# Kernel optimization log

Measured on AMD Instinct MI355X. Metric: run time of the kernel, lower is better.

The kernel has to match this reference:

```python
import jax, jax.numpy as jnp
import numpy as np

UNITS = 128
FILTERS = 32
KSIZE = 31
B, T, DV, DQ = 64, 1000, 512, 1024


def setup_inputs() -> dict:
    key = jax.random.key(0)
    ks = jax.random.split(key, 12)
    scale = 0.05
    inp = {
        "query": jax.random.normal(ks[0], (B, DQ), jnp.float32),
        "values": jax.random.normal(ks[1], (B, T, DV), jnp.float32),
        "previous_attention_weights": jax.random.uniform(ks[2], (B, T, 1), jnp.float32),
        # learned params
        "Wq": jax.random.normal(ks[3], (DQ, UNITS), jnp.float32) * scale,
        "bq": jnp.zeros((UNITS,), jnp.float32),
        "Wm": jax.random.normal(ks[4], (DV, UNITS), jnp.float32) * scale,
        "bm": jnp.zeros((UNITS,), jnp.float32),
        "Wv": jax.random.normal(ks[5], (UNITS, 1), jnp.float32) * scale,
        "bv": jnp.zeros((1,), jnp.float32),
        "Wconv": jax.random.normal(ks[6], (KSIZE, 1, FILTERS), jnp.float32) * scale,  # [W, Cin, Cout]
        "Wl": jax.random.normal(ks[7], (FILTERS, UNITS), jnp.float32) * scale,
    }
    return inp


def _forward(query, values, prev_w, Wq, bq, Wm, bm, Wv, bv, Wconv, Wl):
    # location features: Conv1D (same padding, no bias) then Dense(tanh, no bias)
    loc = jax.lax.conv_general_dilated(
        prev_w, Wconv, window_strides=(1,), padding="SAME",
        dimension_numbers=("NWC", "WIO", "NWC"))          # [B, T, FILTERS]
    loc = jnp.tanh(loc @ Wl)                                # [B, T, UNITS]
    q = query @ Wq + bq                                     # [B, UNITS]
    m = values @ Wm + bm                                    # [B, T, UNITS]
    score = jnp.tanh(m + q[:, None, :] + loc) @ Wv + bv     # [B, T, 1]
    attention_weights = jax.nn.softmax(score, axis=1)       # softmax over time
    context = jnp.sum(attention_weights * values, axis=1)   # [B, DV]
    return context, attention_weights


def reference(query, values, previous_attention_weights, Wq, bq, Wm, bm, Wv, bv, Wconv, Wl):
    return _forward(query, values, previous_attention_weights,
                    Wq, bq, Wm, bm, Wv, bv, Wconv, Wl)
```

## Files before the change

### kernel.cpp

```cpp
#include <hip/hip_runtime.h>

#define B_  64
#define T_  1000
#define DV_ 512
#define DQ_ 1024
#define U_  128
#define F_  32
#define KS_ 31
#define P_  16
#define CT_ 63

typedef __attribute__((ext_vector_type(8))) short short8;
typedef __attribute__((ext_vector_type(4))) float f32x4;

__device__ __forceinline__ unsigned pk2(float a, float b) {
    union { float f; unsigned u; } x, y;
    x.f = a; y.f = b;
    unsigned ra = (x.u + 0x7FFFu + ((x.u >> 16) & 1u)) >> 16;
    unsigned rb = (y.u + 0x7FFFu + ((y.u >> 16) & 1u)) >> 16;
    return (ra & 0xFFFFu) | (rb << 16);
}

__device__ __forceinline__ float fast_tanh(float x) {
    return 1.0f - 2.0f / (__expf(2.0f * x) + 1.0f);
}

__device__ __forceinline__ short8 pk8(float4 f0, float4 f1) {
    int4 q;
    q.x = pk2(f0.x, f0.y); q.y = pk2(f0.z, f0.w);
    q.z = pk2(f1.x, f1.y); q.w = pk2(f1.z, f1.w);
    return *(short8*)&q;
}

__global__ __launch_bounds__(1024) void prep_qb_kernel(
    const float* __restrict__ Wm, const float* __restrict__ Wl,
    const float* __restrict__ query, const float* __restrict__ Wq,
    const float* __restrict__ bq, const float* __restrict__ bm,
    short* __restrict__ WmX, short* __restrict__ WlX, float* __restrict__ qb)
{
    __shared__ float sh[DQ_ + 8 * U_];
    int blk = blockIdx.x, tid = threadIdx.x;
    if (blk < 9) {
        int g = blk * 1024 + tid;
        if (g < 8192) {
            int kc = g >> 9, e = g & 511;
            int n = e >> 2, q = e & 3;
            int kb = kc * 32 + q * 8;
            int4 p;
            p.x = pk2(Wm[(kb + 0) * U_ + n], Wm[(kb + 1) * U_ + n]);
            p.y = pk2(Wm[(kb + 2) * U_ + n], Wm[(kb + 3) * U_ + n]);
            p.z = pk2(Wm[(kb + 4) * U_ + n], Wm[(kb + 5) * U_ + n]);
            p.w = pk2(Wm[(kb + 6) * U_ + n], Wm[(kb + 7) * U_ + n]);
            ((int4*)WmX)[g] = p;
        } else if (g < 8704) {
            int e = g - 8192;
            int n = e >> 2, q = e & 3;
            int kb = q * 8;
            int4 p;
            p.x = pk2(Wl[(kb + 0) * U_ + n], Wl[(kb + 1) * U_ + n]);
            p.y = pk2(Wl[(kb + 2) * U_ + n], Wl[(kb + 3) * U_ + n]);
            p.z = pk2(Wl[(kb + 4) * U_ + n], Wl[(kb + 5) * U_ + n]);
            p.w = pk2(Wl[(kb + 6) * U_ + n], Wl[(kb + 7) * U_ + n]);
            ((int4*)WlX)[e] = p;
        }
    } else {
        float* qs = sh;
        float* red = sh + DQ_;
        int b = blk - 9;
        qs[tid] = query[b * DQ_ + tid];
        __syncthreads();
        int u = tid & 127, p = tid >> 7;
        float a = 0.f;
        const float* wp = Wq + (size_t)p * 128 * U_ + u;
        const float* qp = qs + p * 128;
#pragma unroll 8
        for (int k = 0; k < 128; ++k) a += qp[k] * wp[(size_t)k * U_];
        red[p * U_ + u] = a;
        __syncthreads();
        if (tid < U_) {
            float s = bq[tid] + bm[tid];
#pragma unroll
            for (int pp = 0; pp < 8; ++pp) s += red[pp * U_ + tid];
            qb[b * U_ + tid] = s;
        }
    }
}

__global__ __launch_bounds__(256) void score_kernel(
    const float* __restrict__ values, const float* __restrict__ prev,
    const float* __restrict__ Wc, const float* __restrict__ Wv,
    const float* __restrict__ bv, const short* __restrict__ WmX,
    const short* __restrict__ WlX, const float* __restrict__ qb,
    float* __restrict__ scores)
{
    __shared__ float WcS[KS_ * F_];
    __shared__ short AsL[128 * 32];
    __shared__ float qbS[2 * U_];
    __shared__ float WvS[U_];

    const int tid = threadIdx.x;
    const int r0 = blockIdx.x * 128;
    const int b0 = r0 / T_;
    const int b1 = (r0 + 127) / T_;

    for (int i = tid; i < KS_ * F_; i += 256) WcS[i] = Wc[i];
    if (tid < U_) WvS[tid] = Wv[tid];
    {
        int bb = (tid < U_) ? b0 : b1;
        qbS[tid] = qb[bb * U_ + (tid & (U_ - 1))];
    }

    const int wv = tid >> 6, lane = tid & 63;
    const int quad = lane >> 4, m15 = lane & 15;
    const int row0 = wv * 32 + m15;
    const float* aP0 = values + (size_t)(r0 + row0) * DV_ + quad * 8;
    const float* aP1 = aP0 + (size_t)16 * DV_;
    const int4* bW  = (const int4*)WmX + m15 * 4 + quad;
    const int4* blW = (const int4*)WlX + m15 * 4 + quad;

    float4 aq0[2][2], aq1[2][2], aq2[2][2];
    int4 bf0[8], bf1[8];
    aq0[0][0] = *(const float4*)(aP0);      aq0[0][1] = *(const float4*)(aP0 + 4);
    aq0[1][0] = *(const float4*)(aP1);      aq0[1][1] = *(const float4*)(aP1 + 4);
    aq1[0][0] = *(const float4*)(aP0 + 32); aq1[0][1] = *(const float4*)(aP0 + 36);
    aq1[1][0] = *(const float4*)(aP1 + 32); aq1[1][1] = *(const float4*)(aP1 + 36);
#pragma unroll
    for (int c = 0; c < 8; ++c) bf0[c] = bW[c * 64];

    __syncthreads();

#pragma unroll
    for (int it = 0; it < 2; ++it) {
        int idx = tid + it * 256;
        int i = idx & 127, fg = idx >> 7;
        int r = r0 + i;
        int b = r / T_;
        int t = r - b * T_;
        const float* pv = prev + b * T_;
        float a8[8] = {};
#pragma unroll
        for (int k = 0; k < KS_; ++k) {
            int tt = t + k - 15;
            float p = ((unsigned)tt < (unsigned)T_) ? pv[tt] : 0.f;
#pragma unroll
            for (int j = 0; j < 8; ++j) a8[j] += p * WcS[k * F_ + fg * 8 + j];
        }
        int4 pq;
        pq.x = pk2(a8[0], a8[1]); pq.y = pk2(a8[2], a8[3]);
        pq.z = pk2(a8[4], a8[5]); pq.w = pk2(a8[6], a8[7]);
        ((int4*)AsL)[i * 4 + (fg ^ ((i >> 1) & 3))] = pq;
    }
    __syncthreads();

    f32x4 acc[2][8] = {};
    {
        int row1 = row0 + 16;
        short8 afl0 = ((const short8*)AsL)[row0 * 4 + (quad ^ ((row0 >> 1) & 3))];
        short8 afl1 = ((const short8*)AsL)[row1 * 4 + (quad ^ ((row1 >> 1) & 3))];
#pragma unroll
        for (int c = 0; c < 8; ++c) {
            int4 bl = blW[c * 64];
            acc[0][c] = __builtin_amdgcn_mfma_f32_16x16x32_bf16(afl0, *(short8*)&bl, acc[0][c], 0, 0, 0);
            acc[1][c] = __builtin_amdgcn_mfma_f32_16x16x32_bf16(afl1, *(short8*)&bl, acc[1][c], 0, 0, 0);
        }
        int qoff[2][4];
#pragma unroll
        for (int g = 0; g < 2; ++g)
#pragma unroll
            for (int v = 0; v < 4; ++v) {
                int r = r0 + wv * 32 + g * 16 + quad * 4 + v;
                qoff[g][v] = ((r / T_) == b0) ? 0 : U_;
            }
#pragma unroll
        for (int g = 0; g < 2; ++g)
#pragma unroll
            for (int c = 0; c < 8; ++c) {
                int col = c * 16 + m15;
#pragma unroll
                for (int v = 0; v < 4; ++v)
                    acc[g][c][v] = qbS[qoff[g][v] + col] + fast_tanh(acc[g][c][v]);
            }
    }

#pragma unroll
    for (int kc = 0; kc < 16; ++kc) {
        if (kc + 2 < 16) {
            aq2[0][0] = *(const float4*)(aP0 + (kc + 2) * 32);
            aq2[0][1] = *(const float4*)(aP0 + (kc + 2) * 32 + 4);
            aq2[1][0] = *(const float4*)(aP1 + (kc + 2) * 32);
            aq2[1][1] = *(const float4*)(aP1 + (kc + 2) * 32 + 4);
        }
        if (kc + 1 < 16) {
#pragma unroll
            for (int c = 0; c < 8; ++c) bf1[c] = bW[(kc + 1) * 512 + c * 64];
        }
        short8 af0 = pk8(aq0[0][0], aq0[0][1]);
        short8 af1 = pk8(aq0[1][0], aq0[1][1]);
#pragma unroll
        for (int c = 0; c < 8; ++c) {
            acc[0][c] = __builtin_amdgcn_mfma_f32_16x16x32_bf16(af0, *(short8*)&bf0[c], acc[0][c], 0, 0, 0);
            acc[1][c] = __builtin_amdgcn_mfma_f32_16x16x32_bf16(af1, *(short8*)&bf0[c], acc[1][c], 0, 0, 0);
        }
#pragma unroll
        for (int g = 0; g < 2; ++g) {
            aq0[g][0] = aq1[g][0]; aq0[g][1] = aq1[g][1];
            aq1[g][0] = aq2[g][0]; aq1[g][1] = aq2[g][1];
        }
#pragma unroll
        for (int c = 0; c < 8; ++c) bf0[c] = bf1[c];
    }

    float psum[2][4] = {};
#pragma unroll
    for (int g = 0; g < 2; ++g)
#pragma unroll
        for (int c = 0; c < 8; ++c) {
            int col = c * 16 + m15;
            float wvv = WvS[col];
#pragma unroll
            for (int v = 0; v < 4; ++v)
                psum[g][v] += fast_tanh(acc[g][c][v]) * wvv;
        }
#pragma unroll
    for (int off = 1; off < 16; off <<= 1) {
#pragma unroll
        for (int g = 0; g < 2; ++g)
#pragma unroll
            for (int v = 0; v < 4; ++v) psum[g][v] += __shfl_xor(psum[g][v], off);
    }
    if (m15 == 0) {
        float bvv = bv[0];
#pragma unroll
        for (int g = 0; g < 2; ++g)
#pragma unroll
            for (int v = 0; v < 4; ++v)
                scores[r0 + wv * 32 + g * 16 + quad * 4 + v] = psum[g][v] + bvv;
    }
}

__global__ void softmax_kernel(const float* __restrict__ s, float* __restrict__ w) {
    __shared__ float red[4];
    int b = blockIdx.x, tid = threadIdx.x;
    const float* sb = s + b * T_;
    float v[4];
    int tv[4];
#pragma unroll
    for (int i = 0; i < 4; ++i) {
        int t = tid + i * 256;
        tv[i] = t;
        v[i] = (t < T_) ? sb[t] : -1e30f;
    }
    float mx = fmaxf(fmaxf(v[0], v[1]), fmaxf(v[2], v[3]));
#pragma unroll
    for (int off = 32; off >= 1; off >>= 1) mx = fmaxf(mx, __shfl_xor(mx, off));
    int wv = tid >> 6, lane = tid & 63;
    if (lane == 0) red[wv] = mx;
    __syncthreads();
    mx = fmaxf(fmaxf(red[0], red[1]), fmaxf(red[2], red[3]));
    float e[4];
    float sum = 0.f;
#pragma unroll
    for (int i = 0; i < 4; ++i) {
        e[i] = (tv[i] < T_) ? __expf(v[i] - mx) : 0.f;
        sum += e[i];
    }
#pragma unroll
    for (int off = 32; off >= 1; off >>= 1) sum += __shfl_xor(sum, off);
    __syncthreads();
    if (lane == 0) red[wv] = sum;
    __syncthreads();
    sum = red[0] + red[1] + red[2] + red[3];
    float inv = 1.0f / sum;
#pragma unroll
    for (int i = 0; i < 4; ++i)
        if (tv[i] < T_) w[b * T_ + tv[i]] = e[i] * inv;
}

__global__ __launch_bounds__(256) void ctx1_kernel(
    const float* __restrict__ values, const float* __restrict__ w,
    float* __restrict__ part)
{
    __shared__ float wS[CT_];
    __shared__ float4 ps[128];
    int b = blockIdx.x, p = blockIdx.y, tid = threadIdx.x;
    int t0 = p * CT_;
    int len = (T_ - t0 < CT_) ? (T_ - t0) : CT_;
    if (tid < len) wS[tid] = w[b * T_ + t0 + tid];
    __syncthreads();
    int cl = tid & 127, tp = tid >> 7;
    const float* vp = values + ((size_t)b * T_ + t0) * DV_ + cl * 4;
    float4 a = {0.f, 0.f, 0.f, 0.f};
#pragma unroll 4
    for (int t = tp; t < len; t += 2) {
        float4 v = *(const float4*)(vp + (size_t)t * DV_);
        float wt = wS[t];
        a.x += wt * v.x; a.y += wt * v.y; a.z += wt * v.z; a.w += wt * v.w;
    }
    if (tp == 1) ps[cl] = a;
    __syncthreads();
    if (tp == 0) {
        float4 o = ps[cl];
        o.x += a.x; o.y += a.y; o.z += a.z; o.w += a.w;
        *(float4*)(part + ((size_t)(b * P_ + p)) * DV_ + cl * 4) = o;
    }
}

__global__ void ctx2_kernel(const float* __restrict__ part, float* __restrict__ ctx) {
    int b = blockIdx.x, tid = threadIdx.x;
    const float* pp = part + (size_t)b * P_ * DV_ + tid * 4;
    float4 s = {0.f, 0.f, 0.f, 0.f};
#pragma unroll
    for (int p = 0; p < P_; ++p) {
        float4 v = *(const float4*)(pp + (size_t)p * DV_);
        s.x += v.x; s.y += v.y; s.z += v.z; s.w += v.w;
    }
    *(float4*)(ctx + (size_t)b * DV_ + tid * 4) = s;
}

extern "C" void kernel_launch(void* const* d_in, const int* in_sizes, int n_in,
                              void* d_out, int out_size, void* d_ws, size_t ws_size,
                              hipStream_t stream) {
    const float* query  = (const float*)d_in[0];
    const float* values = (const float*)d_in[1];
    const float* prev   = (const float*)d_in[2];
    const float* Wq     = (const float*)d_in[3];
    const float* bq     = (const float*)d_in[4];
    const float* Wm     = (const float*)d_in[5];
    const float* bm     = (const float*)d_in[6];
    const float* Wv     = (const float*)d_in[7];
    const float* bv     = (const float*)d_in[8];
    const float* Wc     = (const float*)d_in[9];
    const float* Wl     = (const float*)d_in[10];

    float* out  = (float*)d_out;
    float* ctx  = out;
    float* attw = out + B_ * DV_;

    char* ws = (char*)d_ws;
    float* qb     = (float*)(ws);
    float* scores = (float*)(ws + 32768);
    short* WmX    = (short*)(ws + 288768);
    short* WlX    = (short*)(ws + 419840);
    float* part   = (float*)(ws + 428032);

    prep_qb_kernel<<<73, 1024, 0, stream>>>(Wm, Wl, query, Wq, bq, bm, WmX, WlX, qb);
    score_kernel<<<500, 256, 0, stream>>>(values, prev, Wc, Wv, bv, WmX, WlX, qb, scores);
    softmax_kernel<<<B_, 256, 0, stream>>>(scores, attw);
    ctx1_kernel<<<dim3(B_, P_), 256, 0, stream>>>(values, attw, part);
    ctx2_kernel<<<B_, 128, 0, stream>>>(part, ctx);
}
```

Measured before the change: 272.8 us.

## Stage values via global_load_lds double buffer, halve score tile, fuse softmax into context

The score kernel now covers 64 rows per block instead of 128 and runs 1000 blocks with a launch bound of 3 blocks per CU. It streams the values operand into a double-buffered LDS tile with async global_load_lds and a swizzled layout, replacing the per-lane register prefetch. The softmax kernel is folded into the first context kernel: each (batch, chunk) block recomputes the max and sum over all scores, then computes its own weights inline, which removes one launch and one round trip of the weights. The price is redundant softmax reductions in every block, more LDS per block, and a syncthreads each k-step.

```diff
diff --git a/kernel.cpp b/kernel.cpp
--- a/kernel.cpp
+++ b/kernel.cpp
@@ -30,6 +30,12 @@
     q.x = pk2(f0.x, f0.y); q.y = pk2(f0.z, f0.w);
     q.z = pk2(f1.x, f1.y); q.w = pk2(f1.z, f1.w);
     return *(short8*)&q;
+}
+
+__device__ __forceinline__ void gload_lds16(const void* g, void* l) {
+    __builtin_amdgcn_global_load_lds(
+        (const __attribute__((address_space(1))) unsigned*)g,
+        (__attribute__((address_space(3))) unsigned*)l, 16, 0, 0);
 }
 
 __global__ __launch_bounds__(1024) void prep_qb_kernel(
@@ -86,22 +92,46 @@
     }
 }
 
-__global__ __launch_bounds__(256) void score_kernel(
+__global__ __launch_bounds__(256, 3) void score_kernel(
     const float* __restrict__ values, const float* __restrict__ prev,
     const float* __restrict__ Wc, const float* __restrict__ Wv,
     const float* __restrict__ bv, const short* __restrict__ WmX,
     const short* __restrict__ WlX, const float* __restrict__ qb,
     float* __restrict__ scores)
 {
+    __shared__ float As[2][64 * 64];
+    __shared__ short AsL[64 * 32];
     __shared__ float WcS[KS_ * F_];
-    __shared__ short AsL[128 * 32];
     __shared__ float qbS[2 * U_];
     __shared__ float WvS[U_];
 
     const int tid = threadIdx.x;
-    const int r0 = blockIdx.x * 128;
+    const int r0 = blockIdx.x * 64;
     const int b0 = r0 / T_;
-    const int b1 = (r0 + 127) / T_;
+    const int b1 = (r0 + 63) / T_;
+
+    const int wv = tid >> 6, lane = tid & 63;
+    const int quad = lane >> 4, m15 = lane & 15;
+    const int esw = (m15 & 3) << 1;
+    const int lrow = lane >> 4;
+    const int lunit = (lane & 15) ^ (lrow << 1);
+
+    const int4* bW  = (const int4*)WmX + m15 * 4 + quad;
+    const int4* blW = (const int4*)WlX + m15 * 4 + quad;
+
+    auto stage = [&](int buf, int k0) {
+#pragma unroll
+        for (int j = 0; j < 4; ++j) {
+            const float* src = values + (size_t)(r0 + wv * 16 + j * 4 + lrow) * DV_
+                               + k0 + lunit * 4;
+            gload_lds16(src, &As[buf][(wv * 16 + j * 4) * 64]);
+        }
+    };
+
+    stage(0, 0);
+    int4 bfA[8], bfB[8];
+#pragma unroll
+    for (int c = 0; c < 8; ++c) bfA[c] = bW[c * 64];
 
     for (int i = tid; i < KS_ * F_; i += 256) WcS[i] = Wc[i];
     if (tid < U_) WvS[tid] = Wv[tid];
@@ -109,30 +139,10 @@
         int bb = (tid < U_) ? b0 : b1;
         qbS[tid] = qb[bb * U_ + (tid & (U_ - 1))];
     }
-
-    const int wv = tid >> 6, lane = tid & 63;
-    const int quad = lane >> 4, m15 = lane & 15;
-    const int row0 = wv * 32 + m15;
-    const float* aP0 = values + (size_t)(r0 + row0) * DV_ + quad * 8;
-    const float* aP1 = aP0 + (size_t)16 * DV_;
-    const int4* bW  = (const int4*)WmX + m15 * 4 + quad;
-    const int4* blW = (const int4*)WlX + m15 * 4 + quad;
-
-    float4 aq0[2][2], aq1[2][2], aq2[2][2];
-    int4 bf0[8], bf1[8];
-    aq0[0][0] = *(const float4*)(aP0);      aq0[0][1] = *(const float4*)(aP0 + 4);
-    aq0[1][0] = *(const float4*)(aP1);      aq0[1][1] = *(const float4*)(aP1 + 4);
-    aq1[0][0] = *(const float4*)(aP0 + 32); aq1[0][1] = *(const float4*)(aP0 + 36);
-    aq1[1][0] = *(const float4*)(aP1 + 32); aq1[1][1] = *(const float4*)(aP1 + 36);
-#pragma unroll
-    for (int c = 0; c < 8; ++c) bf0[c] = bW[c * 64];
-
-    __syncthreads();
-
-#pragma unroll
-    for (int it = 0; it < 2; ++it) {
-        int idx = tid + it * 256;
-        int i = idx & 127, fg = idx >> 7;
+    __syncthreads();
+
+    {
+        int i = tid & 63, fg = tid >> 6;
         int r = r0 + i;
         int b = r / T_;
         int t = r - b * T_;
@@ -152,149 +162,132 @@
     }
     __syncthreads();
 
-    f32x4 acc[2][8] = {};
+    const int row = wv * 16 + m15;
+    f32x4 acc[8] = {};
     {
-        int row1 = row0 + 16;
-        short8 afl0 = ((const short8*)AsL)[row0 * 4 + (quad ^ ((row0 >> 1) & 3))];
-        short8 afl1 = ((const short8*)AsL)[row1 * 4 + (quad ^ ((row1 >> 1) & 3))];
+        short8 afl = ((const short8*)AsL)[row * 4 + (quad ^ ((row >> 1) & 3))];
 #pragma unroll
         for (int c = 0; c < 8; ++c) {
             int4 bl = blW[c * 64];
-            acc[0][c] = __builtin_amdgcn_mfma_f32_16x16x32_bf16(afl0, *(short8*)&bl, acc[0][c], 0, 0, 0);
-            acc[1][c] = __builtin_amdgcn_mfma_f32_16x16x32_bf16(afl1, *(short8*)&bl, acc[1][c], 0, 0, 0);
-        }
-        int qoff[2][4];
-#pragma unroll
-        for (int g = 0; g < 2; ++g)
-#pragma unroll
-            for (int v = 0; v < 4; ++v) {
-                int r = r0 + wv * 32 + g * 16 + quad * 4 + v;
-                qoff[g][v] = ((r / T_) == b0) ? 0 : U_;
-            }
-#pragma unroll
-        for (int g = 0; g < 2; ++g)
-#pragma unroll
-            for (int c = 0; c < 8; ++c) {
-                int col = c * 16 + m15;
-#pragma unroll
-                for (int v = 0; v < 4; ++v)
-                    acc[g][c][v] = qbS[qoff[g][v] + col] + fast_tanh(acc[g][c][v]);
-            }
-    }
-
-#pragma unroll
-    for (int kc = 0; kc < 16; ++kc) {
-        if (kc + 2 < 16) {
-            aq2[0][0] = *(const float4*)(aP0 + (kc + 2) * 32);
-            aq2[0][1] = *(const float4*)(aP0 + (kc + 2) * 32 + 4);
-            aq2[1][0] = *(const float4*)(aP1 + (kc + 2) * 32);
-            aq2[1][1] = *(const float4*)(aP1 + (kc + 2) * 32 + 4);
-        }
-        if (kc + 1 < 16) {
-#pragma unroll
-            for (int c = 0; c < 8; ++c) bf1[c] = bW[(kc + 1) * 512 + c * 64];
-        }
-        short8 af0 = pk8(aq0[0][0], aq0[0][1]);
-        short8 af1 = pk8(aq0[1][0], aq0[1][1]);
-#pragma unroll
-        for (int c = 0; c < 8; ++c) {
-            acc[0][c] = __builtin_amdgcn_mfma_f32_16x16x32_bf16(af0, *(short8*)&bf0[c], acc[0][c], 0, 0, 0);
-            acc[1][c] = __builtin_amdgcn_mfma_f32_16x16x32_bf16(af1, *(short8*)&bf0[c], acc[1][c], 0, 0, 0);
-        }
-#pragma unroll
-        for (int g = 0; g < 2; ++g) {
-            aq0[g][0] = aq1[g][0]; aq0[g][1] = aq1[g][1];
-            aq1[g][0] = aq2[g][0]; aq1[g][1] = aq2[g][1];
-        }
-#pragma unroll
-        for (int c = 0; c < 8; ++c) bf0[c] = bf1[c];
-    }
-
-    float psum[2][4] = {};
-#pragma unroll
-    for (int g = 0; g < 2; ++g)
+            acc[c] = __builtin_amdgcn_mfma_f32_16x16x32_bf16(afl, *(short8*)&bl, acc[c], 0, 0, 0);
+        }
+        int qoff[4];
+#pragma unroll
+        for (int v = 0; v < 4; ++v) {
+            int r = r0 + wv * 16 + quad * 4 + v;
+            qoff[v] = ((r / T_) == b0) ? 0 : U_;
+        }
 #pragma unroll
         for (int c = 0; c < 8; ++c) {
             int col = c * 16 + m15;
-            float wvv = WvS[col];
 #pragma unroll
             for (int v = 0; v < 4; ++v)
-                psum[g][v] += fast_tanh(acc[g][c][v]) * wvv;
-        }
+                acc[c][v] = qbS[qoff[v] + col] + fast_tanh(acc[c][v]);
+        }
+    }
+    __syncthreads();
+
+#pragma unroll
+    for (int s = 0; s < 8; ++s) {
+        if (s + 1 < 8) stage((s + 1) & 1, (s + 1) * 64);
+#pragma unroll
+        for (int c = 0; c < 8; ++c) bfB[c] = bW[(2 * s + 1) * 512 + c * 64];
+
+        const float4* ap = (const float4*)&As[s & 1][row * 64];
+        {
+            int u0 = (2 * quad) ^ esw;
+            float4 f0 = ap[u0], f1 = ap[u0 + 1];
+            short8 af = pk8(f0, f1);
+#pragma unroll
+            for (int c = 0; c < 8; ++c)
+                acc[c] = __builtin_amdgcn_mfma_f32_16x16x32_bf16(af, *(short8*)&bfB[0] == *(short8*)&bfB[0] ? *(short8*)&bfA[c] : *(short8*)&bfA[c], acc[c], 0, 0, 0);
+        }
+        int4 bfN[8];
+        if (s + 1 < 8) {
+#pragma unroll
+            for (int c = 0; c < 8; ++c) bfN[c] = bW[(2 * s + 2) * 512 + c * 64];
+        }
+        {
+            int u0 = (2 * (4 + quad)) ^ esw;
+            float4 f0 = ap[u0], f1 = ap[u0 + 1];
+            short8 af = pk8(f0, f1);
+#pragma unroll
+            for (int c = 0; c < 8; ++c)
+                acc[c] = __builtin_amdgcn_mfma_f32_16x16x32_bf16(af, *(short8*)&bfB[c], acc[c], 0, 0, 0);
+        }
+#pragma unroll
+        for (int c = 0; c < 8; ++c) bfA[c] = bfN[c];
+        __syncthreads();
+    }
+
+    float psum[4] = {0.f, 0.f, 0.f, 0.f};
+#pragma unroll
+    for (int c = 0; c < 8; ++c) {
+        int col = c * 16 + m15;
+        float wvv = WvS[col];
+#pragma unroll
+        for (int v = 0; v < 4; ++v)
+            psum[v] += fast_tanh(acc[c][v]) * wvv;
+    }
 #pragma unroll
     for (int off = 1; off < 16; off <<= 1) {
 #pragma unroll
-        for (int g = 0; g < 2; ++g)
-#pragma unroll
-            for (int v = 0; v < 4; ++v) psum[g][v] += __shfl_xor(psum[g][v], off);
+        for (int v = 0; v < 4; ++v) psum[v] += __shfl_xor(psum[v], off);
     }
     if (m15 == 0) {
         float bvv = bv[0];
 #pragma unroll
-        for (int g = 0; g < 2; ++g)
-#pragma unroll
-            for (int v = 0; v < 4; ++v)
-                scores[r0 + wv * 32 + g * 16 + quad * 4 + v] = psum[g][v] + bvv;
-    }
-}
-
-__global__ void softmax_kernel(const float* __restrict__ s, float* __restrict__ w) {
+        for (int v = 0; v < 4; ++v)
+            scores[r0 + wv * 16 + quad * 4 + v] = psum[v] + bvv;
+    }
+}
+
+__global__ __launch_bounds__(256) void ctxsm_kernel(
+    const float* __restrict__ scores, const float* __restrict__ values,
+    float* __restrict__ attw, float* __restrict__ part)
+{
+    __shared__ float sS[1024];
     __shared__ float red[4];
-    int b = blockIdx.x, tid = threadIdx.x;
-    const float* sb = s + b * T_;
+    __shared__ float4 ps[128];
+    int b = blockIdx.x, p = blockIdx.y, tid = threadIdx.x;
+    const float* sb = scores + b * T_;
     float v[4];
-    int tv[4];
 #pragma unroll
     for (int i = 0; i < 4; ++i) {
         int t = tid + i * 256;
-        tv[i] = t;
         v[i] = (t < T_) ? sb[t] : -1e30f;
+        sS[t] = v[i];
     }
     float mx = fmaxf(fmaxf(v[0], v[1]), fmaxf(v[2], v[3]));
 #pragma unroll
     for (int off = 32; off >= 1; off >>= 1) mx = fmaxf(mx, __shfl_xor(mx, off));
-    int wv = tid >> 6, lane = tid & 63;
-    if (lane == 0) red[wv] = mx;
+    int wvi = tid >> 6, lane = tid & 63;
+    if (lane == 0) red[wvi] = mx;
     __syncthreads();
     mx = fmaxf(fmaxf(red[0], red[1]), fmaxf(red[2], red[3]));
-    float e[4];
     float sum = 0.f;
 #pragma unroll
-    for (int i = 0; i < 4; ++i) {
-        e[i] = (tv[i] < T_) ? __expf(v[i] - mx) : 0.f;
-        sum += e[i];
-    }
+    for (int i = 0; i < 4; ++i)
+        sum += (tid + i * 256 < T_) ? __expf(v[i] - mx) : 0.f;
 #pragma unroll
     for (int off = 32; off >= 1; off >>= 1) sum += __shfl_xor(sum, off);
     __syncthreads();
-    if (lane == 0) red[wv] = sum;
-    __syncthreads();
-    sum = red[0] + red[1] + red[2] + red[3];
-    float inv = 1.0f / sum;
-#pragma unroll
-    for (int i = 0; i < 4; ++i)
-        if (tv[i] < T_) w[b * T_ + tv[i]] = e[i] * inv;
-}
-
-__global__ __launch_bounds__(256) void ctx1_kernel(
-    const float* __restrict__ values, const float* __restrict__ w,
-    float* __restrict__ part)
-{
-    __shared__ float wS[CT_];
-    __shared__ float4 ps[128];
-    int b = blockIdx.x, p = blockIdx.y, tid = threadIdx.x;
+    if (lane == 0) red[wvi] = sum;
+    __syncthreads();
+    float inv = 1.0f / (red[0] + red[1] + red[2] + red[3]);
+
     int t0 = p * CT_;
     int len = (T_ - t0 < CT_) ? (T_ - t0) : CT_;
-    if (tid < len) wS[tid] = w[b * T_ + t0 + tid];
-    __syncthreads();
+    if (tid < len) attw[b * T_ + t0 + tid] = __expf(sS[t0 + tid] - mx) * inv;
+
     int cl = tid & 127, tp = tid >> 7;
     const float* vp = values + ((size_t)b * T_ + t0) * DV_ + cl * 4;
     float4 a = {0.f, 0.f, 0.f, 0.f};
 #pragma unroll 4
     for (int t = tp; t < len; t += 2) {
-        float4 v = *(const float4*)(vp + (size_t)t * DV_);
-        float wt = wS[t];
-        a.x += wt * v.x; a.y += wt * v.y; a.z += wt * v.z; a.w += wt * v.w;
+        float4 vv = *(const float4*)(vp + (size_t)t * DV_);
+        float wt = __expf(sS[t0 + t] - mx) * inv;
+        a.x += wt * vv.x; a.y += wt * vv.y; a.z += wt * vv.z; a.w += wt * vv.w;
     }
     if (tp == 1) ps[cl] = a;
     __syncthreads();
@@ -344,8 +337,7 @@
     float* part   = (float*)(ws + 428032);
 
     prep_qb_kernel<<<73, 1024, 0, stream>>>(Wm, Wl, query, Wq, bq, bm, WmX, WlX, qb);
-    score_kernel<<<500, 256, 0, stream>>>(values, prev, Wc, Wv, bv, WmX, WlX, qb, scores);
-    softmax_kernel<<<B_, 256, 0, stream>>>(scores, attw);
-    ctx1_kernel<<<dim3(B_, P_), 256, 0, stream>>>(values, attw, part);
+    score_kernel<<<1000, 256, 0, stream>>>(values, prev, Wc, Wv, bv, WmX, WlX, qb, scores);
+    ctxsm_kernel<<<dim3(B_, P_), 256, 0, stream>>>(scores, values, attw, part);
     ctx2_kernel<<<B_, 128, 0, stream>>>(part, ctx);
 }
```

Result: slower. 323.8 us (+18.7%).
